# Performance work log

Measured on AMD Instinct MI355X. Metric: run time of the kernel, lower is better.

Reference implementation:

```python
import jax, jax.numpy as jnp
import numpy as np


def setup_inputs() -> dict:
    key = jax.random.key(0)
    k1, k2 = jax.random.split(key)
    x = jax.random.normal(k1, (32, 64, 32, 32), dtype=jnp.float32)
    codebook = jax.random.normal(k2, (2048, 64), dtype=jnp.float32)
    return {"x": x, "codebook": codebook}


def reference(x, codebook):
    B, C, H, W = x.shape
    # (B, C, H, W) -> (B*H*W, C) channels-last flatten
    xf = jnp.transpose(x, (0, 2, 3, 1)).reshape(-1, C)
    d2 = (jnp.sum(xf * xf, axis=-1, keepdims=True)
          + jnp.sum(codebook * codebook, axis=-1)[None, :]
          - 2.0 * jnp.einsum('nc,kc->nk', xf, codebook))
    idx = jnp.argmin(d2, axis=-1)            # (B*H*W,)
    quant = codebook[idx]                    # (B*H*W, C)
    commitment_loss = jnp.mean((jax.lax.stop_gradient(quant) - xf) ** 2)
    codebook_loss = jnp.mean((quant - jax.lax.stop_gradient(xf)) ** 2)
    # Straight-through estimator
    quant_ste = xf + jax.lax.stop_gradient(quant - xf)
    quant_out = jnp.transpose(quant_ste.reshape(B, H, W, C), (0, 3, 1, 2))
    min_encoding_indices = idx.reshape(B, H, W)
    return quant_out, codebook_loss, commitment_loss, min_encoding_indices
```

## Files before the change

kernel.cpp:

```cpp
#include <hip/hip_runtime.h>

#define NROWS    32768
#define KENT     2048
#define OUT_Q_SZ 2097152
#define N_ELEMS  2097152.0f
#define THR      1e-4f
#define KLO      0.001953125f

typedef _Float16 f16x8  __attribute__((ext_vector_type(8)));
typedef float    f32x16 __attribute__((ext_vector_type(16)));

#define WS_LOSS  0
#define WS_CNT   4
#define WS_EN    1024
#define WS_LIST  16384
#define WS_CBH   262144
#define WS_CBL   524288

__global__ __launch_bounds__(256) void vq_prep_kernel(
    const float* __restrict__ cb, float* __restrict__ ws)
{
    const int unit = blockIdx.x * 256 + threadIdx.x;
    if (unit == 0) { ws[0] = 0.0f; ((unsigned*)ws)[1] = 0u; }

    const int gm = unit >> 8, ks = (unit >> 6) & 3, l = unit & 63;
    const int e  = gm * 32 + (l & 31);
    const int ch = ks * 16 + ((l >> 5) << 3);
    float4 v0 = *(const float4*)(cb + e * 64 + ch);
    float4 v1 = *(const float4*)(cb + e * 64 + ch + 4);
    float vv[8] = {v0.x, v0.y, v0.z, v0.w, v1.x, v1.y, v1.z, v1.w};
    f16x8 h, lo;
#pragma unroll
    for (int j = 0; j < 8; ++j) {
        _Float16 hi = (_Float16)vv[j];
        float r = (vv[j] - (float)hi) * 1024.0f;
        h[j] = hi; lo[j] = (_Float16)r;
    }
    *(f16x8*)((_Float16*)((char*)ws + WS_CBH) + unit * 8) = h;
    *(f16x8*)((_Float16*)((char*)ws + WS_CBL) + unit * 8) = lo;

    if (unit < KENT) {
        const float4* row = (const float4*)(cb + unit * 64);
        float s = 0.0f;
#pragma unroll
        for (int i = 0; i < 16; ++i) {
            float4 v = row[i];
            s += v.x * v.x + v.y * v.y + v.z * v.z + v.w * v.w;
        }
        *((float*)((char*)ws + WS_EN) + unit) = s;
    }
}

__global__ __launch_bounds__(512, 4) void vq_main_kernel(
    const float* __restrict__ x, const float* __restrict__ cb,
    float* __restrict__ ws, float* __restrict__ out_q,
    float* __restrict__ out_idx)
{
    __shared__ float lds_x[64 * 68];
    __shared__ float mb1[64 * 4];
    __shared__ float mb2[64 * 4];
    __shared__ int   mbi[64 * 4];
    __shared__ int   idx_s[64];
    __shared__ int   flag_s[64];
    __shared__ float wp[8];

    const float*    en  = (const float*)((char*)ws + WS_EN);
    const _Float16* cbh = (const _Float16*)((char*)ws + WS_CBH);
    const _Float16* cbl = (const _Float16*)((char*)ws + WS_CBL);
    unsigned* cnt  = (unsigned*)((char*)ws + WS_CNT);
    unsigned* list = (unsigned*)((char*)ws + WS_LIST);

    const int tid = threadIdx.x;
    const int n0  = blockIdx.x * 64;
    const int b   = n0 >> 10;
    const int hw0 = n0 & 1023;
    const float* xg = x + b * 65536 + hw0;

    {
        int c = tid >> 3, s = tid & 7;
        float4 a0 = *(const float4*)(xg + c * 1024 + s * 8);
        float4 a1 = *(const float4*)(xg + c * 1024 + s * 8 + 4);
        *(float4*)(&lds_x[c * 68 + s * 8])     = a0;
        *(float4*)(&lds_x[c * 68 + s * 8 + 4]) = a1;
    }
    __syncthreads();

    const int l  = tid & 63;
    const int wv = tid >> 6;
    const int rh = wv >> 2;
    const int eq = wv & 3;
    const int r0 = rh * 32;

    f16x8 bh[4], bl[4];
#pragma unroll
    for (int ks = 0; ks < 4; ++ks) {
        f16x8 h, lo;
#pragma unroll
        for (int j = 0; j < 8; ++j) {
            int ch = ks * 16 + ((l >> 5) << 3) + j;
            float f = lds_x[ch * 68 + r0 + (l & 31)];
            _Float16 hi = (_Float16)f;
            float r = (f - (float)hi) * 1024.0f;
            h[j] = hi; lo[j] = (_Float16)r;
        }
        bh[ks] = h; bl[ks] = lo;
    }

    float m1 = 3.4e38f, m2 = 3.4e38f;
    int   bix = 0;
    const int lane_eoff = (l >> 5) << 2;

#pragma unroll 1
    for (int m = 0; m < 16; ++m) {
        const int gm = eq * 16 + m;
        const _Float16* ap = cbh + ((size_t)(gm * 4) * 64 + l) * 8;
        const _Float16* lp = cbl + ((size_t)(gm * 4) * 64 + l) * 8;
        f16x8 ah0 = *(const f16x8*)(ap);
        f16x8 ah1 = *(const f16x8*)(ap + 512);
        f16x8 ah2 = *(const f16x8*)(ap + 1024);
        f16x8 ah3 = *(const f16x8*)(ap + 1536);
        f16x8 al0 = *(const f16x8*)(lp);
        f16x8 al1 = *(const f16x8*)(lp + 512);
        f16x8 al2 = *(const f16x8*)(lp + 1024);
        f16x8 al3 = *(const f16x8*)(lp + 1536);

        f32x16 z = {0.f,0.f,0.f,0.f,0.f,0.f,0.f,0.f,0.f,0.f,0.f,0.f,0.f,0.f,0.f,0.f};
        f32x16 acch = __builtin_amdgcn_mfma_f32_32x32x16_f16(ah0, bh[0], z, 0, 0, 0);
        acch = __builtin_amdgcn_mfma_f32_32x32x16_f16(ah1, bh[1], acch, 0, 0, 0);
        acch = __builtin_amdgcn_mfma_f32_32x32x16_f16(ah2, bh[2], acch, 0, 0, 0);
        acch = __builtin_amdgcn_mfma_f32_32x32x16_f16(ah3, bh[3], acch, 0, 0, 0);
        f32x16 accl = __builtin_amdgcn_mfma_f32_32x32x16_f16(ah0, bl[0], z, 0, 0, 0);
        accl = __builtin_amdgcn_mfma_f32_32x32x16_f16(ah1, bl[1], accl, 0, 0, 0);
        accl = __builtin_amdgcn_mfma_f32_32x32x16_f16(ah2, bl[2], accl, 0, 0, 0);
        accl = __builtin_amdgcn_mfma_f32_32x32x16_f16(ah3, bl[3], accl, 0, 0, 0);
        accl = __builtin_amdgcn_mfma_f32_32x32x16_f16(al0, bh[0], accl, 0, 0, 0);
        accl = __builtin_amdgcn_mfma_f32_32x32x16_f16(al1, bh[1], accl, 0, 0, 0);
        accl = __builtin_amdgcn_mfma_f32_32x32x16_f16(al2, bh[2], accl, 0, 0, 0);
        accl = __builtin_amdgcn_mfma_f32_32x32x16_f16(al3, bh[3], accl, 0, 0, 0);

        const int ebase = eq * 512 + m * 32 + lane_eoff;
        const float* ep = en + ebase;
        float4 e0 = *(const float4*)(ep);
        float4 e1 = *(const float4*)(ep + 8);
        float4 e2 = *(const float4*)(ep + 16);
        float4 e3 = *(const float4*)(ep + 24);
        float ev[16] = {e0.x,e0.y,e0.z,e0.w, e1.x,e1.y,e1.z,e1.w,
                        e2.x,e2.y,e2.z,e2.w, e3.x,e3.y,e3.z,e3.w};

#pragma unroll
        for (int r = 0; r < 16; ++r) {
            float d = fmaf(acch[r], -2.0f, fmaf(accl[r], -KLO, ev[r]));
            bool lt = d < m1;
            m2 = __builtin_amdgcn_fmed3f(d, m1, m2);
            m1 = fminf(d, m1);
            bix = lt ? (ebase + ((r >> 2) << 3) + (r & 3)) : bix;
        }
    }

    {
        float o1 = __shfl_xor(m1, 32, 64);
        float o2 = __shfl_xor(m2, 32, 64);
        int   oi = __shfl_xor(bix, 32, 64);
        bool lt = (o1 < m1) || (o1 == m1 && oi < bix);
        float loser = lt ? m1 : o1;
        m1 = lt ? o1 : m1; bix = lt ? oi : bix;
        m2 = fminf(loser, fminf(m2, o2));
    }
    if (l < 32) {
        int row = r0 + l;
        mb1[row * 4 + eq] = m1;
        mb2[row * 4 + eq] = m2;
        mbi[row * 4 + eq] = bix;
    }
    __syncthreads();

    if (tid < 64) {
        float v1 = 3.4e38f, v2 = 3.4e38f; int ix = 0;
#pragma unroll
        for (int q = 0; q < 4; ++q) {
            float o1 = mb1[tid * 4 + q];
            float o2 = mb2[tid * 4 + q];
            int   oi = mbi[tid * 4 + q];
            bool lt = (o1 < v1) || (o1 == v1 && oi < ix);
            float loser = lt ? v1 : o1;
            v1 = lt ? o1 : v1; ix = lt ? oi : ix;
            v2 = fminf(loser, fminf(v2, o2));
        }
        out_idx[n0 + tid] = (float)ix;
        int fl = (v2 - v1) <= THR;
        idx_s[tid] = ix; flag_s[tid] = fl;
        if (fl) { unsigned p = atomicAdd(cnt, 1u); list[p] = n0 + tid; }
    }
    __syncthreads();

    float lsum = 0.0f;
#pragma unroll
    for (int it = 0; it < 8; ++it) {
        int e = it * 512 + tid;
        int c = e >> 6, r = e & 63;
        float q  = cb[idx_s[r] * 64 + c];
        float xv = lds_x[c * 68 + r];
        out_q[(b << 16) + (c << 10) + hw0 + r] = xv + (q - xv);
        float df = q - xv;
        lsum += flag_s[r] ? 0.0f : df * df;
    }
#pragma unroll
    for (int mm = 1; mm < 64; mm <<= 1) lsum += __shfl_xor(lsum, mm, 64);
    if (l == 0) wp[wv] = lsum;
    __syncthreads();
    if (tid == 0) {
        float s = 0.0f;
#pragma unroll
        for (int w = 0; w < 8; ++w) s += wp[w];
        atomicAdd((float*)ws, s);
    }
}

__global__ __launch_bounds__(256) void vq_fallback_kernel(
    const float* __restrict__ x, const float* __restrict__ cb,
    float* __restrict__ ws, float* __restrict__ out_q, float* __restrict__ out_idx)
{
    __shared__ float x_s[64];
    __shared__ float rd[256];
    __shared__ int   ri[256];

    const float* en = (const float*)((char*)ws + WS_EN);
    const unsigned F = *(const unsigned*)((char*)ws + WS_CNT);
    const unsigned* list = (const unsigned*)((char*)ws + WS_LIST);
    const int t = threadIdx.x;

    for (unsigned li = blockIdx.x; li < F; li += gridDim.x) {
        int row = list[li];
        int b = row >> 10, hw = row & 1023;
        if (t < 64) x_s[t] = x[(b << 16) + (t << 10) + hw];
        __syncthreads();

        float best = 3.4e38f; int bi = 0;
#pragma unroll 1
        for (int i = 0; i < 8; ++i) {
            int e = i * 256 + t;
            float dot = 0.0f;
#pragma unroll
            for (int c4 = 0; c4 < 16; ++c4) {
                float4 cv = *(const float4*)(cb + e * 64 + c4 * 4);
                float4 xv = *(const float4*)&x_s[c4 * 4];
                dot += cv.x * xv.x + cv.y * xv.y + cv.z * xv.z + cv.w * xv.w;
            }
            float d = en[e] - 2.0f * dot;
            if (d < best) { best = d; bi = e; }
        }
        rd[t] = best; ri[t] = bi;
        __syncthreads();
        for (int s = 128; s > 0; s >>= 1) {
            if (t < s) {
                bool lt = (rd[t + s] < rd[t]) || (rd[t + s] == rd[t] && ri[t + s] < ri[t]);
                if (lt) { rd[t] = rd[t + s]; ri[t] = ri[t + s]; }
            }
            __syncthreads();
        }
        int ix = ri[0];
        if (t == 0) out_idx[row] = (float)ix;
        if (t < 64) {
            float q = cb[ix * 64 + t];
            float xv = x_s[t];
            out_q[(b << 16) + (t << 10) + hw] = xv + (q - xv);
            float df = q - xv;
            float lsum = df * df;
#pragma unroll
            for (int mm = 1; mm < 64; mm <<= 1) lsum += __shfl_xor(lsum, mm, 64);
            if (t == 0) atomicAdd((float*)ws, lsum);
        }
        __syncthreads();
    }
}

__global__ void vq_finalize_kernel(const float* __restrict__ ws, float* __restrict__ out) {
    float m = ws[0] * (1.0f / N_ELEMS);
    out[OUT_Q_SZ]     = m;
    out[OUT_Q_SZ + 1] = m;
}

extern "C" void kernel_launch(void* const* d_in, const int* in_sizes, int n_in,
                              void* d_out, int out_size, void* d_ws, size_t ws_size,
                              hipStream_t stream) {
    const float* x  = (const float*)d_in[0];
    const float* cb = (const float*)d_in[1];
    float* out = (float*)d_out;
    float* ws  = (float*)d_ws;

    vq_prep_kernel<<<64, 256, 0, stream>>>(cb, ws);
    vq_main_kernel<<<512, 512, 0, stream>>>(x, cb, ws, out, out + OUT_Q_SZ + 2);
    vq_fallback_kernel<<<64, 256, 0, stream>>>(x, cb, ws, out, out + OUT_Q_SZ + 2);
    vq_finalize_kernel<<<1, 1, 0, stream>>>(ws, out);
}
```

Measured before the change: 68.85 us.

## Process two row tiles per wave and fold codebook norms into MFMA init

Each block of the main kernel now covers 128 rows instead of 64, and each wave runs two 32-row MFMA tiles against the same codebook fragments. This halves codebook fragment loads per row, at the cost of more registers and half as many blocks. The squared codebook norms are pre-scaled by -0.5 and pre-permuted in the prep kernel so they can seed the MFMA accumulator, which turns the search into an argmax with fewer per-element ops. The running best and second-best values are split into four independent chains per tile to shorten dependency chains. The near-tie threshold now applies to the halved score, so slightly more rows may be sent to the exact fallback kernel.

```diff
diff --git a/kernel.cpp b/kernel.cpp
--- a/kernel.cpp
+++ b/kernel.cpp
@@ -4,16 +4,15 @@
 #define KENT     2048
 #define OUT_Q_SZ 2097152
 #define N_ELEMS  2097152.0f
-#define THR      1e-4f
-#define KLO      0.001953125f
+#define THRG     1e-4f
+#define KLO      0.0009765625f
 
 typedef _Float16 f16x8  __attribute__((ext_vector_type(8)));
 typedef float    f32x16 __attribute__((ext_vector_type(16)));
 
-#define WS_LOSS  0
-#define WS_CNT   4
 #define WS_EN    1024
-#define WS_LIST  16384
+#define WS_ENH   9216
+#define WS_LIST  20480
 #define WS_CBH   262144
 #define WS_CBL   524288
 
@@ -28,7 +27,7 @@
     const int ch = ks * 16 + ((l >> 5) << 3);
     float4 v0 = *(const float4*)(cb + e * 64 + ch);
     float4 v1 = *(const float4*)(cb + e * 64 + ch + 4);
-    float vv[8] = {v0.x, v0.y, v0.z, v0.w, v1.x, v1.y, v1.z, v1.w};
+    float vv[8] = {v0.x,v0.y,v0.z,v0.w, v1.x,v1.y,v1.z,v1.w};
     f16x8 h, lo;
 #pragma unroll
     for (int j = 0; j < 8; ++j) {
@@ -36,8 +35,8 @@
         float r = (vv[j] - (float)hi) * 1024.0f;
         h[j] = hi; lo[j] = (_Float16)r;
     }
-    *(f16x8*)((_Float16*)((char*)ws + WS_CBH) + unit * 8) = h;
-    *(f16x8*)((_Float16*)((char*)ws + WS_CBL) + unit * 8) = lo;
+    *(f16x8*)((_Float16*)((char*)ws + WS_CBH) + (size_t)unit * 8) = h;
+    *(f16x8*)((_Float16*)((char*)ws + WS_CBL) + (size_t)unit * 8) = lo;
 
     if (unit < KENT) {
         const float4* row = (const float4*)(cb + unit * 64);
@@ -48,73 +47,78 @@
             s += v.x * v.x + v.y * v.y + v.z * v.z + v.w * v.w;
         }
         *((float*)((char*)ws + WS_EN) + unit) = s;
-    }
-}
-
-__global__ __launch_bounds__(512, 4) void vq_main_kernel(
+        int ein = unit & 31;
+        int half = (ein >> 2) & 1;
+        int r = (ein & 3) + ((ein >> 3) << 2);
+        *((float*)((char*)ws + WS_ENH) + (unit & ~31) + half * 16 + r) = -0.5f * s;
+    }
+}
+
+__global__ __launch_bounds__(512, 2) void vq_main_kernel(
     const float* __restrict__ x, const float* __restrict__ cb,
     float* __restrict__ ws, float* __restrict__ out_q,
     float* __restrict__ out_idx)
 {
-    __shared__ float lds_x[64 * 68];
-    __shared__ float mb1[64 * 4];
-    __shared__ float mb2[64 * 4];
-    __shared__ int   mbi[64 * 4];
-    __shared__ int   idx_s[64];
-    __shared__ int   flag_s[64];
+    __shared__ float lds_x[64 * 132];
+    __shared__ float mb1[128 * 4], mb2[128 * 4];
+    __shared__ int   mbi[128 * 4];
+    __shared__ int   idx_s[128], flag_s[128];
     __shared__ float wp[8];
 
-    const float*    en  = (const float*)((char*)ws + WS_EN);
-    const _Float16* cbh = (const _Float16*)((char*)ws + WS_CBH);
-    const _Float16* cbl = (const _Float16*)((char*)ws + WS_CBL);
-    unsigned* cnt  = (unsigned*)((char*)ws + WS_CNT);
+    const float*    enhp = (const float*)((char*)ws + WS_ENH);
+    const _Float16* cbh  = (const _Float16*)((char*)ws + WS_CBH);
+    const _Float16* cbl  = (const _Float16*)((char*)ws + WS_CBL);
+    unsigned* cnt  = (unsigned*)ws + 1;
     unsigned* list = (unsigned*)((char*)ws + WS_LIST);
 
-    const int tid = threadIdx.x;
-    const int n0  = blockIdx.x * 64;
+    const int tid = threadIdx.x, bid = blockIdx.x;
+    const int n0  = bid * 128;
     const int b   = n0 >> 10;
     const int hw0 = n0 & 1023;
     const float* xg = x + b * 65536 + hw0;
 
-    {
-        int c = tid >> 3, s = tid & 7;
-        float4 a0 = *(const float4*)(xg + c * 1024 + s * 8);
-        float4 a1 = *(const float4*)(xg + c * 1024 + s * 8 + 4);
-        *(float4*)(&lds_x[c * 68 + s * 8])     = a0;
-        *(float4*)(&lds_x[c * 68 + s * 8 + 4]) = a1;
+#pragma unroll
+    for (int it = 0; it < 4; ++it) {
+        int f = it * 512 + tid;
+        int c = f >> 5, seg = f & 31;
+        float4 v = *(const float4*)(xg + c * 1024 + seg * 4);
+        *(float4*)(&lds_x[c * 132 + seg * 4]) = v;
     }
     __syncthreads();
 
-    const int l  = tid & 63;
-    const int wv = tid >> 6;
-    const int rh = wv >> 2;
-    const int eq = wv & 3;
-    const int r0 = rh * 32;
-
-    f16x8 bh[4], bl[4];
-#pragma unroll
-    for (int ks = 0; ks < 4; ++ks) {
-        f16x8 h, lo;
-#pragma unroll
-        for (int j = 0; j < 8; ++j) {
-            int ch = ks * 16 + ((l >> 5) << 3) + j;
-            float f = lds_x[ch * 68 + r0 + (l & 31)];
-            _Float16 hi = (_Float16)f;
-            float r = (f - (float)hi) * 1024.0f;
-            h[j] = hi; lo[j] = (_Float16)r;
-        }
-        bh[ks] = h; bl[ks] = lo;
-    }
-
-    float m1 = 3.4e38f, m2 = 3.4e38f;
-    int   bix = 0;
-    const int lane_eoff = (l >> 5) << 2;
-
-#pragma unroll 1
+    const int l   = tid & 63;
+    const int wv  = tid >> 6;
+    const int rgp = wv >> 2;
+    const int eq  = wv & 3;
+    const int r0  = rgp * 64;
+
+    f16x8 bh[2][4], bl[2][4];
+#pragma unroll
+    for (int s = 0; s < 2; ++s)
+#pragma unroll
+        for (int ks = 0; ks < 4; ++ks) {
+            f16x8 h, lo;
+#pragma unroll
+            for (int j = 0; j < 8; ++j) {
+                int ch = ks * 16 + ((l >> 5) << 3) + j;
+                float f = lds_x[ch * 132 + r0 + s * 32 + (l & 31)];
+                _Float16 hi = (_Float16)f;
+                float r = (f - (float)hi) * 1024.0f;
+                h[j] = hi; lo[j] = (_Float16)r;
+            }
+            bh[s][ks] = h; bl[s][ks] = lo;
+        }
+
+    float m1[2][4], m2[2][4]; int bx[2][4];
+#pragma unroll
+    for (int s = 0; s < 2; ++s)
+#pragma unroll
+        for (int t = 0; t < 4; ++t) { m1[s][t] = -3.4e38f; m2[s][t] = -3.4e38f; bx[s][t] = 0; }
+
+#pragma unroll 2
     for (int m = 0; m < 16; ++m) {
-        const int gm = eq * 16 + m;
-        const _Float16* ap = cbh + ((size_t)(gm * 4) * 64 + l) * 8;
-        const _Float16* lp = cbl + ((size_t)(gm * 4) * 64 + l) * 8;
+        const _Float16* ap = cbh + ((size_t)((eq * 16 + m) * 4) * 64 + l) * 8;
+        const _Float16* lp = cbl + ((size_t)((eq * 16 + m) * 4) * 64 + l) * 8;
         f16x8 ah0 = *(const f16x8*)(ap);
         f16x8 ah1 = *(const f16x8*)(ap + 512);
         f16x8 ah2 = *(const f16x8*)(ap + 1024);
@@ -124,70 +128,103 @@
         f16x8 al2 = *(const f16x8*)(lp + 1024);
         f16x8 al3 = *(const f16x8*)(lp + 1536);
 
-        f32x16 z = {0.f,0.f,0.f,0.f,0.f,0.f,0.f,0.f,0.f,0.f,0.f,0.f,0.f,0.f,0.f,0.f};
-        f32x16 acch = __builtin_amdgcn_mfma_f32_32x32x16_f16(ah0, bh[0], z, 0, 0, 0);
-        acch = __builtin_amdgcn_mfma_f32_32x32x16_f16(ah1, bh[1], acch, 0, 0, 0);
-        acch = __builtin_amdgcn_mfma_f32_32x32x16_f16(ah2, bh[2], acch, 0, 0, 0);
-        acch = __builtin_amdgcn_mfma_f32_32x32x16_f16(ah3, bh[3], acch, 0, 0, 0);
-        f32x16 accl = __builtin_amdgcn_mfma_f32_32x32x16_f16(ah0, bl[0], z, 0, 0, 0);
-        accl = __builtin_amdgcn_mfma_f32_32x32x16_f16(ah1, bl[1], accl, 0, 0, 0);
-        accl = __builtin_amdgcn_mfma_f32_32x32x16_f16(ah2, bl[2], accl, 0, 0, 0);
-        accl = __builtin_amdgcn_mfma_f32_32x32x16_f16(ah3, bl[3], accl, 0, 0, 0);
-        accl = __builtin_amdgcn_mfma_f32_32x32x16_f16(al0, bh[0], accl, 0, 0, 0);
-        accl = __builtin_amdgcn_mfma_f32_32x32x16_f16(al1, bh[1], accl, 0, 0, 0);
-        accl = __builtin_amdgcn_mfma_f32_32x32x16_f16(al2, bh[2], accl, 0, 0, 0);
-        accl = __builtin_amdgcn_mfma_f32_32x32x16_f16(al3, bh[3], accl, 0, 0, 0);
-
-        const int ebase = eq * 512 + m * 32 + lane_eoff;
-        const float* ep = en + ebase;
-        float4 e0 = *(const float4*)(ep);
-        float4 e1 = *(const float4*)(ep + 8);
-        float4 e2 = *(const float4*)(ep + 16);
-        float4 e3 = *(const float4*)(ep + 24);
-        float ev[16] = {e0.x,e0.y,e0.z,e0.w, e1.x,e1.y,e1.z,e1.w,
-                        e2.x,e2.y,e2.z,e2.w, e3.x,e3.y,e3.z,e3.w};
-
+        f32x16 aA;
+        {
+            const float4* ep4 = (const float4*)(enhp + eq * 512 + m * 32 + ((l >> 5) << 4));
+            float4 q0 = ep4[0], q1 = ep4[1], q2 = ep4[2], q3 = ep4[3];
+            aA[0]=q0.x; aA[1]=q0.y; aA[2]=q0.z; aA[3]=q0.w;
+            aA[4]=q1.x; aA[5]=q1.y; aA[6]=q1.z; aA[7]=q1.w;
+            aA[8]=q2.x; aA[9]=q2.y; aA[10]=q2.z; aA[11]=q2.w;
+            aA[12]=q3.x; aA[13]=q3.y; aA[14]=q3.z; aA[15]=q3.w;
+        }
+        f32x16 aB = aA;
+        f32x16 cA = {0.f,0.f,0.f,0.f,0.f,0.f,0.f,0.f,0.f,0.f,0.f,0.f,0.f,0.f,0.f,0.f};
+        f32x16 cB = cA;
+
+        aA = __builtin_amdgcn_mfma_f32_32x32x16_f16(ah0, bh[0][0], aA, 0, 0, 0);
+        aB = __builtin_amdgcn_mfma_f32_32x32x16_f16(ah0, bh[1][0], aB, 0, 0, 0);
+        cA = __builtin_amdgcn_mfma_f32_32x32x16_f16(ah0, bl[0][0], cA, 0, 0, 0);
+        cB = __builtin_amdgcn_mfma_f32_32x32x16_f16(ah0, bl[1][0], cB, 0, 0, 0);
+        aA = __builtin_amdgcn_mfma_f32_32x32x16_f16(ah1, bh[0][1], aA, 0, 0, 0);
+        aB = __builtin_amdgcn_mfma_f32_32x32x16_f16(ah1, bh[1][1], aB, 0, 0, 0);
+        cA = __builtin_amdgcn_mfma_f32_32x32x16_f16(ah1, bl[0][1], cA, 0, 0, 0);
+        cB = __builtin_amdgcn_mfma_f32_32x32x16_f16(ah1, bl[1][1], cB, 0, 0, 0);
+        aA = __builtin_amdgcn_mfma_f32_32x32x16_f16(ah2, bh[0][2], aA, 0, 0, 0);
+        aB = __builtin_amdgcn_mfma_f32_32x32x16_f16(ah2, bh[1][2], aB, 0, 0, 0);
+        cA = __builtin_amdgcn_mfma_f32_32x32x16_f16(ah2, bl[0][2], cA, 0, 0, 0);
+        cB = __builtin_amdgcn_mfma_f32_32x32x16_f16(ah2, bl[1][2], cB, 0, 0, 0);
+        aA = __builtin_amdgcn_mfma_f32_32x32x16_f16(ah3, bh[0][3], aA, 0, 0, 0);
+        aB = __builtin_amdgcn_mfma_f32_32x32x16_f16(ah3, bh[1][3], aB, 0, 0, 0);
+        cA = __builtin_amdgcn_mfma_f32_32x32x16_f16(ah3, bl[0][3], cA, 0, 0, 0);
+        cB = __builtin_amdgcn_mfma_f32_32x32x16_f16(ah3, bl[1][3], cB, 0, 0, 0);
+        cA = __builtin_amdgcn_mfma_f32_32x32x16_f16(al0, bh[0][0], cA, 0, 0, 0);
+        cB = __builtin_amdgcn_mfma_f32_32x32x16_f16(al0, bh[1][0], cB, 0, 0, 0);
+        cA = __builtin_amdgcn_mfma_f32_32x32x16_f16(al1, bh[0][1], cA, 0, 0, 0);
+        cB = __builtin_amdgcn_mfma_f32_32x32x16_f16(al1, bh[1][1], cB, 0, 0, 0);
+        cA = __builtin_amdgcn_mfma_f32_32x32x16_f16(al2, bh[0][2], cA, 0, 0, 0);
+        cB = __builtin_amdgcn_mfma_f32_32x32x16_f16(al2, bh[1][2], cB, 0, 0, 0);
+        cA = __builtin_amdgcn_mfma_f32_32x32x16_f16(al3, bh[0][3], cA, 0, 0, 0);
+        cB = __builtin_amdgcn_mfma_f32_32x32x16_f16(al3, bh[1][3], cB, 0, 0, 0);
+
+        const int ebl = eq * 512 + m * 32 + ((l >> 5) << 2);
 #pragma unroll
         for (int r = 0; r < 16; ++r) {
-            float d = fmaf(acch[r], -2.0f, fmaf(accl[r], -KLO, ev[r]));
-            bool lt = d < m1;
-            m2 = __builtin_amdgcn_fmed3f(d, m1, m2);
-            m1 = fminf(d, m1);
-            bix = lt ? (ebase + ((r >> 2) << 3) + (r & 3)) : bix;
-        }
-    }
-
-    {
-        float o1 = __shfl_xor(m1, 32, 64);
-        float o2 = __shfl_xor(m2, 32, 64);
-        int   oi = __shfl_xor(bix, 32, 64);
-        bool lt = (o1 < m1) || (o1 == m1 && oi < bix);
-        float loser = lt ? m1 : o1;
-        m1 = lt ? o1 : m1; bix = lt ? oi : bix;
-        m2 = fminf(loser, fminf(m2, o2));
-    }
-    if (l < 32) {
-        int row = r0 + l;
-        mb1[row * 4 + eq] = m1;
-        mb2[row * 4 + eq] = m2;
-        mbi[row * 4 + eq] = bix;
+            int t = r >> 2;
+            int ent = ebl + ((r >> 2) << 3) + (r & 3);
+            float gA = fmaf(cA[r], KLO, aA[r]);
+            bool  tA = gA > m1[0][t];
+            m2[0][t] = __builtin_amdgcn_fmed3f(gA, m1[0][t], m2[0][t]);
+            m1[0][t] = fmaxf(gA, m1[0][t]);
+            bx[0][t] = tA ? ent : bx[0][t];
+            float gB = fmaf(cB[r], KLO, aB[r]);
+            bool  tB = gB > m1[1][t];
+            m2[1][t] = __builtin_amdgcn_fmed3f(gB, m1[1][t], m2[1][t]);
+            m1[1][t] = fmaxf(gB, m1[1][t]);
+            bx[1][t] = tB ? ent : bx[1][t];
+        }
+    }
+
+#pragma unroll
+    for (int s = 0; s < 2; ++s) {
+        float v1 = m1[s][0], v2 = m2[s][0]; int ix = bx[s][0];
+#pragma unroll
+        for (int t = 1; t < 4; ++t) {
+            bool gt = (m1[s][t] > v1) || (m1[s][t] == v1 && bx[s][t] < ix);
+            float loser = gt ? v1 : m1[s][t];
+            v1 = gt ? m1[s][t] : v1;
+            ix = gt ? bx[s][t] : ix;
+            v2 = fmaxf(loser, fmaxf(v2, m2[s][t]));
+        }
+        float o1 = __shfl_xor(v1, 32, 64);
+        float o2 = __shfl_xor(v2, 32, 64);
+        int   oi = __shfl_xor(ix, 32, 64);
+        bool gt = (o1 > v1) || (o1 == v1 && oi < ix);
+        float loser = gt ? v1 : o1;
+        v1 = gt ? o1 : v1; ix = gt ? oi : ix;
+        v2 = fmaxf(loser, fmaxf(v2, o2));
+        if (l < 32) {
+            int row = r0 + s * 32 + l;
+            mb1[row * 4 + eq] = v1;
+            mb2[row * 4 + eq] = v2;
+            mbi[row * 4 + eq] = ix;
+        }
     }
     __syncthreads();
 
-    if (tid < 64) {
-        float v1 = 3.4e38f, v2 = 3.4e38f; int ix = 0;
+    if (tid < 128) {
+        float v1 = -3.4e38f, v2 = -3.4e38f; int ix = 0;
 #pragma unroll
         for (int q = 0; q < 4; ++q) {
             float o1 = mb1[tid * 4 + q];
             float o2 = mb2[tid * 4 + q];
             int   oi = mbi[tid * 4 + q];
-            bool lt = (o1 < v1) || (o1 == v1 && oi < ix);
-            float loser = lt ? v1 : o1;
-            v1 = lt ? o1 : v1; ix = lt ? oi : ix;
-            v2 = fminf(loser, fminf(v2, o2));
+            bool gt = (o1 > v1) || (o1 == v1 && oi < ix);
+            float loser = gt ? v1 : o1;
+            v1 = gt ? o1 : v1; ix = gt ? oi : ix;
+            v2 = fmaxf(loser, fmaxf(v2, o2));
         }
         out_idx[n0 + tid] = (float)ix;
-        int fl = (v2 - v1) <= THR;
+        int fl = (v1 - v2) <= THRG;
         idx_s[tid] = ix; flag_s[tid] = fl;
         if (fl) { unsigned p = atomicAdd(cnt, 1u); list[p] = n0 + tid; }
     }
@@ -195,11 +232,11 @@
 
     float lsum = 0.0f;
 #pragma unroll
-    for (int it = 0; it < 8; ++it) {
+    for (int it = 0; it < 16; ++it) {
         int e = it * 512 + tid;
-        int c = e >> 6, r = e & 63;
+        int c = e >> 7, r = e & 127;
         float q  = cb[idx_s[r] * 64 + c];
-        float xv = lds_x[c * 68 + r];
+        float xv = lds_x[c * 132 + r];
         out_q[(b << 16) + (c << 10) + hw0 + r] = xv + (q - xv);
         float df = q - xv;
         lsum += flag_s[r] ? 0.0f : df * df;
@@ -212,7 +249,7 @@
         float s = 0.0f;
 #pragma unroll
         for (int w = 0; w < 8; ++w) s += wp[w];
-        atomicAdd((float*)ws, s);
+        atomicAdd(ws, s);
     }
 }
 
@@ -225,7 +262,7 @@
     __shared__ int   ri[256];
 
     const float* en = (const float*)((char*)ws + WS_EN);
-    const unsigned F = *(const unsigned*)((char*)ws + WS_CNT);
+    const unsigned F = *(const unsigned*)((char*)ws + 4);
     const unsigned* list = (const unsigned*)((char*)ws + WS_LIST);
     const int t = threadIdx.x;
 
@@ -253,7 +290,8 @@
         __syncthreads();
         for (int s = 128; s > 0; s >>= 1) {
             if (t < s) {
-                bool lt = (rd[t + s] < rd[t]) || (rd[t + s] == rd[t] && ri[t + s] < ri[t]);
+                bool lt = (rd[t + s] < rd[t]) ||
+                          (rd[t + s] == rd[t] && ri[t + s] < ri[t]);
                 if (lt) { rd[t] = rd[t + s]; ri[t] = ri[t + s]; }
             }
             __syncthreads();
@@ -265,10 +303,10 @@
             float xv = x_s[t];
             out_q[(b << 16) + (t << 10) + hw] = xv + (q - xv);
             float df = q - xv;
-            float lsum = df * df;
-#pragma unroll
-            for (int mm = 1; mm < 64; mm <<= 1) lsum += __shfl_xor(lsum, mm, 64);
-            if (t == 0) atomicAdd((float*)ws, lsum);
+            float ls = df * df;
+#pragma unroll
+            for (int mm = 1; mm < 64; mm <<= 1) ls += __shfl_xor(ls, mm, 64);
+            if (t == 0) atomicAdd(ws, ls);
         }
         __syncthreads();
     }
@@ -285,11 +323,12 @@
                               hipStream_t stream) {
     const float* x  = (const float*)d_in[0];
     const float* cb = (const float*)d_in[1];
-    float* out = (float*)d_out;
-    float* ws  = (float*)d_ws;
+    float* out  = (float*)d_out;
+    float* ws   = (float*)d_ws;
+    float* oidx = out + OUT_Q_SZ + 2;
 
     vq_prep_kernel<<<64, 256, 0, stream>>>(cb, ws);
-    vq_main_kernel<<<512, 512, 0, stream>>>(x, cb, ws, out, out + OUT_Q_SZ + 2);
-    vq_fallback_kernel<<<64, 256, 0, stream>>>(x, cb, ws, out, out + OUT_Q_SZ + 2);
+    vq_main_kernel<<<256, 512, 0, stream>>>(x, cb, ws, out, oidx);
+    vq_fallback_kernel<<<64, 256, 0, stream>>>(x, cb, ws, out, oidx);
     vq_finalize_kernel<<<1, 1, 0, stream>>>(ws, out);
 }
```

Result: no change. 68.10 us (-1.1%).
